# Kernel optimization log

Measured on AMD Instinct MI355X. Metric: run time of the kernel, lower is better.

Reference implementation:

```python
import jax, jax.numpy as jnp
import numpy as np

N = 50000
E = 1600000
D = 64


def setup_inputs() -> dict:
    key = jax.random.key(0)
    ks = jax.random.split(key, 12)
    glorot = lambda k, shape: jax.random.uniform(
        k, shape, jnp.float32, -1.0, 1.0) * (np.sqrt(2.0) * np.sqrt(6.0 / sum(shape)))
    return {
        "feat": jax.random.normal(ks[0], (N, D), jnp.float32),
        "norm": jax.random.uniform(ks[1], (N,), jnp.float32),
        "edge_src": jax.random.randint(ks[2], (E,), 0, N),
        "edge_dst": jax.random.randint(ks[3], (E,), 0, N),
        "etype": jax.random.randint(ks[4], (E,), 0, 4),
        "W_rel": glorot(ks[5], (D, D)),
        "lin_w": glorot(ks[6], (2 * D, 1)),
        "lin_b": jnp.zeros((1,), jnp.float32),
        "loop_w": glorot(ks[7], (D, D)),
        "evolve_loop_w": glorot(ks[8], (D, D)),
    }


def reference(feat, norm, edge_src, edge_dst, etype, W_rel, lin_w, lin_b,
              loop_w, evolve_loop_w):
    # --- message function: per-edge attention + per-edge matmul ---
    src = feat[edge_src]              # [E, D] gather
    dst = feat[edge_dst]              # [E, D] gather
    att_logit = jnp.concatenate([src, dst], axis=1) @ lin_w + lin_b  # [E, 1]
    atten = jax.nn.sigmoid(jax.nn.relu(att_logit[:, 0]))            # [E]
    # source code applies weight_relation to every edge-type bucket, so the
    # etype split+concat is a no-op permutation of messages
    msg = src @ W_rel                                                # [E, D]

    # --- reduce: attention-weighted mailbox sum (segment reduction) ---
    agg = jax.ops.segment_sum(atten[:, None] * msg, edge_dst, num_segments=N)
    indeg = jax.ops.segment_sum(jnp.ones((edge_dst.shape[0],), feat.dtype),
                                edge_dst, num_segments=N)            # [N]
    has_msg = (indeg > 0)[:, None]
    # DGL: zero in-degree nodes keep their old feat; apply_func scales by norm
    node_feat = jnp.where(has_msg, agg, feat) * norm[:, None]

    # --- self loop: loop_weight where in_degree>0, evolve_loop_weight else ---
    loop_msg = jnp.where(has_msg, feat @ loop_w, feat @ evolve_loop_w)

    return jnp.tanh(node_feat + loop_msg)
```

## Files before the change

### kernel.cpp

```cpp
#include <hip/hip_runtime.h>
#include <hip/hip_bf16.h>
#include <hip/hip_fp16.h>
#include <math.h>


#define D 64
#define SHIFT 6
#define NB (1 << SHIFT)
#define SCM 1024
#define CHUNK 4096
#define CAPB 2560
#define NPW 8

typedef _Float16 half8 __attribute__((ext_vector_type(8)));
typedef float f32x4 __attribute__((ext_vector_type(4)));

__global__ __launch_bounds__(256) void fused_pre(
    const float* __restrict__ feat, const float* __restrict__ W_rel,
    const float* __restrict__ lin_w, const float* __restrict__ lin_b,
    const float* __restrict__ loop_w, const float* __restrict__ evolve_w,
    float* __restrict__ s1, float* __restrict__ s2, __half* __restrict__ FWh,
    __half* __restrict__ WT, int N) {
  if (blockIdx.x == 0) {
    for (int i = threadIdx.x; i < 192 * 64; i += 256) {
      const int c192 = i >> 6, k = i & 63;
      const int m = c192 >> 6, c = c192 & 63;
      const float* Wm = (m == 0) ? W_rel : (m == 1) ? loop_w : evolve_w;
      WT[i] = __float2half(Wm[k * 64 + c]);
    }
  }

  const int lane = threadIdx.x & 63;
  const int w    = threadIdx.x >> 6;
  const int r    = lane & 15;
  const int g    = lane >> 4;
  const int m0   = (blockIdx.x * 4 + w) * 16;
  if (m0 >= N) return;

  half8 bw[4][2];
  half8 ba[2];
  #pragma unroll
  for (int ks = 0; ks < 2; ++ks) {
    #pragma unroll
    for (int j = 0; j < 8; ++j) {
      const int k = ks * 32 + g * 8 + j;
      #pragma unroll
      for (int nt = 0; nt < 4; ++nt)
        bw[nt][ks][j] = (_Float16)W_rel[k * 64 + nt * 16 + r];
      const float av = (r == 0) ? lin_w[k] : (r == 1) ? lin_w[64 + k] : 0.0f;
      ba[ks][j] = (_Float16)av;
    }
  }

  half8 ah[2], al[2];
  const int arow = m0 + r;
  #pragma unroll
  for (int ks = 0; ks < 2; ++ks) {
    float v[8];
    if (arow < N) {
      const float4 u0 = *(const float4*)&feat[(size_t)arow * D + ks * 32 + g * 8];
      const float4 u1 = *(const float4*)&feat[(size_t)arow * D + ks * 32 + g * 8 + 4];
      v[0] = u0.x; v[1] = u0.y; v[2] = u0.z; v[3] = u0.w;
      v[4] = u1.x; v[5] = u1.y; v[6] = u1.z; v[7] = u1.w;
    } else {
      #pragma unroll
      for (int q = 0; q < 8; ++q) v[q] = 0.0f;
    }
    #pragma unroll
    for (int q = 0; q < 8; ++q) {
      const _Float16 hh = (_Float16)v[q];
      ah[ks][q] = hh;
      al[ks][q] = (_Float16)(v[q] - (float)hh);
    }
  }

  #pragma unroll
  for (int nt = 0; nt < 4; ++nt) {
    f32x4 acc = {0.0f, 0.0f, 0.0f, 0.0f};
    #pragma unroll
    for (int ks = 0; ks < 2; ++ks) {
      acc = __builtin_amdgcn_mfma_f32_16x16x32_f16(ah[ks], bw[nt][ks], acc, 0, 0, 0);
      acc = __builtin_amdgcn_mfma_f32_16x16x32_f16(al[ks], bw[nt][ks], acc, 0, 0, 0);
    }
    #pragma unroll
    for (int q = 0; q < 4; ++q) {
      const int n = m0 + g * 4 + q;
      if (n < N) FWh[(size_t)n * D + nt * 16 + r] = __float2half(acc[q]);
    }
  }

  f32x4 acc5 = {0.0f, 0.0f, 0.0f, 0.0f};
  #pragma unroll
  for (int ks = 0; ks < 2; ++ks) {
    acc5 = __builtin_amdgcn_mfma_f32_16x16x32_f16(ah[ks], ba[ks], acc5, 0, 0, 0);
    acc5 = __builtin_amdgcn_mfma_f32_16x16x32_f16(al[ks], ba[ks], acc5, 0, 0, 0);
  }
  if (r < 2) {
    const float b = lin_b[0];
    #pragma unroll
    for (int q = 0; q < 4; ++q) {
      const int n = m0 + g * 4 + q;
      if (n < N) {
        if (r == 0) s1[n] = acc5[q] + b;
        else        s2[n] = acc5[q];
      }
    }
  }
}

__global__ __launch_bounds__(512) void coarse_scatter(
    const int* __restrict__ esrc, const int* __restrict__ edst,
    const float* __restrict__ s1, const float* __restrict__ s2,
    int* __restrict__ gcur, uint2* __restrict__ ebuf, int E, int C) {
  __shared__ int h[SCM];
  __shared__ int cur[SCM];
  __shared__ int bl[SCM];
  for (int i = threadIdx.x; i < C; i += 512) h[i] = 0;
  __syncthreads();
  const int E4 = E >> 2;
  const int4* edst4 = (const int4*)edst;
  const int4* esrc4 = (const int4*)esrc;
  const int b4 = blockIdx.x * (CHUNK >> 2);
  const bool tail0 = (blockIdx.x == 0) && (threadIdx.x == 0);

  #pragma unroll
  for (int k = 0; k < CHUNK / 2048; ++k) {
    const int i4 = b4 + threadIdx.x + 512 * k;
    if (i4 < E4) {
      const int4 d = edst4[i4];
      atomicAdd(&h[d.x >> SHIFT], 1);
      atomicAdd(&h[d.y >> SHIFT], 1);
      atomicAdd(&h[d.z >> SHIFT], 1);
      atomicAdd(&h[d.w >> SHIFT], 1);
    }
  }
  if (tail0) for (int e = E4 << 2; e < E; ++e) atomicAdd(&h[edst[e] >> SHIFT], 1);
  __syncthreads();
  for (int i = threadIdx.x; i < C; i += 512) {
    const int v = h[i];
    bl[i] = v ? atomicAdd(&gcur[i], v) : 0;
    cur[i] = 0;
  }
  __syncthreads();

  #pragma unroll
  for (int k = 0; k < CHUNK / 2048; ++k) {
    const int i4 = b4 + threadIdx.x + 512 * k;
    if (i4 < E4) {
      const int4 s = esrc4[i4];
      const int4 d = edst4[i4];
      const int ss[4] = {s.x, s.y, s.z, s.w};
      const int dd[4] = {d.x, d.y, d.z, d.w};
      float a1[4], a2[4];
      #pragma unroll
      for (int j = 0; j < 4; ++j) a1[j] = s1[ss[j]];
      #pragma unroll
      for (int j = 0; j < 4; ++j) a2[j] = s2[dd[j]];
      #pragma unroll
      for (int j = 0; j < 4; ++j) {
        const float a = 1.0f / (1.0f + __expf(-fmaxf(a1[j] + a2[j], 0.0f)));
        const int bk = dd[j] >> SHIFT;
        const int rr = atomicAdd(&cur[bk], 1);
        ebuf[(size_t)bk * CAPB + bl[bk] + rr] =
            make_uint2((unsigned)ss[j] | ((unsigned)(dd[j] & (NB - 1)) << 26),
                       __float_as_uint(a));
      }
    }
  }
  if (tail0) {
    for (int e = E4 << 2; e < E; ++e) {
      const int sj = esrc[e], dj = edst[e];
      const float a = 1.0f / (1.0f + __expf(-fmaxf(s1[sj] + s2[dj], 0.0f)));
      const int bk = dj >> SHIFT;
      const int rr = atomicAdd(&cur[bk], 1);
      ebuf[(size_t)bk * CAPB + bl[bk] + rr] =
          make_uint2((unsigned)sj | ((unsigned)(dj & (NB - 1)) << 26),
                     __float_as_uint(a));
    }
  }
}

__global__ __launch_bounds__(512, 4) void sort_reduce_finalize(
    const float* __restrict__ feat, const __half* __restrict__ FWh,
    const __half* __restrict__ WT, const float* __restrict__ norm,
    const int* __restrict__ gcur, const uint2* __restrict__ ebuf,
    float* __restrict__ out, int C, int N) {
  __shared__ uint2 sdata[CAPB];
  __shared__ float Yl[NB * D];
  __shared__ int hist[NB];
  __shared__ int starts[NB + 1];
  __shared__ int roff[NB];

  const int tid  = threadIdx.x;
  const int lane = tid & 63;
  const int w    = tid >> 6;
  const int b    = blockIdx.x;
  const int n0   = b << SHIFT;
  const int beg  = b * CAPB;
  const int cnt  = min(gcur[b], CAPB);

  if (tid < NB) hist[tid] = 0;
  __syncthreads();

  uint2 ereg[5];
  #pragma unroll
  for (int k = 0; k < 5; ++k) {
    const int i = tid + (k << 9);
    if (i < cnt) ereg[k] = ebuf[beg + i];
  }

  const int r = lane & 15, g = lane >> 4;
  const bool evw = (w >= 4);
  const int mt = w & 3;
  f32x4 ym[4];
  {
    half8 ah[2], al[2];
    const int arow = n0 + mt * 16 + r;
    #pragma unroll
    for (int ks = 0; ks < 2; ++ks) {
      float v[8];
      if (arow < N) {
        const float4 u0 = *(const float4*)&feat[(size_t)arow * D + ks * 32 + g * 8];
        const float4 u1 = *(const float4*)&feat[(size_t)arow * D + ks * 32 + g * 8 + 4];
        v[0] = u0.x; v[1] = u0.y; v[2] = u0.z; v[3] = u0.w;
        v[4] = u1.x; v[5] = u1.y; v[6] = u1.z; v[7] = u1.w;
      } else {
        #pragma unroll
        for (int q = 0; q < 8; ++q) v[q] = 0.0f;
      }
      #pragma unroll
      for (int q = 0; q < 8; ++q) {
        const _Float16 hh = (_Float16)v[q];
        ah[ks][q] = hh;
        al[ks][q] = (_Float16)(v[q] - (float)hh);
      }
    }
    const int wrow0 = evw ? 128 : 64;
    #pragma unroll
    for (int nt = 0; nt < 4; ++nt) {
      f32x4 a0 = {0.0f, 0.0f, 0.0f, 0.0f};
      #pragma unroll
      for (int ks = 0; ks < 2; ++ks) {
        const half8 bw = *reinterpret_cast<const half8*>(
            WT + (size_t)(wrow0 + nt * 16 + r) * 64 + ks * 32 + g * 8);
        a0 = __builtin_amdgcn_mfma_f32_16x16x32_f16(ah[ks], bw, a0, 0, 0, 0);
        a0 = __builtin_amdgcn_mfma_f32_16x16x32_f16(al[ks], bw, a0, 0, 0, 0);
      }
      ym[nt] = a0;
    }
  }

  #pragma unroll
  for (int k = 0; k < 5; ++k) {
    const int i = tid + (k << 9);
    if (i < cnt) atomicAdd(&hist[ereg[k].x >> 26], 1);
  }
  __syncthreads();
  if (tid < 64) {
    const int v = hist[tid];
    int incl = v;
    #pragma unroll
    for (int off = 1; off < 64; off <<= 1) {
      const int o = __shfl_up(incl, off, 64);
      if (tid >= off) incl += o;
    }
    starts[tid] = incl - v;
    roff[tid]   = incl - v;
    if (tid == 63) starts[64] = incl;
  }
  __syncthreads();
  #pragma unroll
  for (int k = 0; k < 5; ++k) {
    const int i = tid + (k << 9);
    if (i < cnt) {
      const int pos = atomicAdd(&roff[ereg[k].x >> 26], 1);
      sdata[pos] = ereg[k];
    }
  }
  #pragma unroll
  for (int nt = 0; nt < 4; ++nt) {
    #pragma unroll
    for (int q = 0; q < 4; ++q) {
      const int gr = mt * 16 + g * 4 + q;
      const bool hm = starts[gr + 1] > starts[gr];
      if (evw != hm) Yl[gr * D + nt * 16 + r] = ym[nt][q];
    }
  }
  __syncthreads();

  float agg[NPW];
  #pragma unroll
  for (int j = 0; j < NPW; ++j) agg[j] = 0.0f;
  for (int j = 0; j < NPW; ++j) {
    const int dl = w * NPW + j;
    const int n  = n0 + dl;
    if (n >= N) break;
    const int rb = __builtin_amdgcn_readfirstlane(starts[dl]);
    const int re = __builtin_amdgcn_readfirstlane(starts[dl + 1]);
    float a = 0.0f;
    int p = rb;
    for (; p + 16 <= re; p += 16) {
      uint2 ee[16];
      #pragma unroll
      for (int q = 0; q < 16; ++q) ee[q] = sdata[p + q];
      float ff[16];
      #pragma unroll
      for (int q = 0; q < 16; ++q)
        ff[q] = __half2float(FWh[(size_t)(ee[q].x & 0x03FFFFFFu) * D + lane]);
      #pragma unroll
      for (int q = 0; q < 16; ++q) a += __uint_as_float(ee[q].y) * ff[q];
    }
    for (; p + 4 <= re; p += 4) {
      uint2 ee[4];
      #pragma unroll
      for (int q = 0; q < 4; ++q) ee[q] = sdata[p + q];
      #pragma unroll
      for (int q = 0; q < 4; ++q)
        a += __uint_as_float(ee[q].y) *
             __half2float(FWh[(size_t)(ee[q].x & 0x03FFFFFFu) * D + lane]);
    }
    for (; p < re; ++p) {
      const uint2 en = sdata[p];
      a += __uint_as_float(en.y) *
           __half2float(FWh[(size_t)(en.x & 0x03FFFFFFu) * D + lane]);
    }
    agg[j] = a;
  }

  for (int j = 0; j < NPW; ++j) {
    const int dl = w * NPW + j;
    const int n  = n0 + dl;
    if (n >= N) break;
    const bool hm = starts[dl + 1] > starts[dl];
    const float nr = norm[n];
    const float base = hm ? agg[j] : feat[(size_t)n * D + lane];
    out[(size_t)n * D + lane] = tanhf(base * nr + Yl[dl * D + lane]);
  }
}

extern "C" void kernel_launch(void* const* d_in, const int* in_sizes, int n_in,
                              void* d_out, int out_size, void* d_ws, size_t ws_size,
                              hipStream_t stream) {
  const float* feat     = (const float*)d_in[0];
  const float* norm     = (const float*)d_in[1];
  const int*   esrc     = (const int*)d_in[2];
  const int*   edst     = (const int*)d_in[3];
  const float* W_rel    = (const float*)d_in[5];
  const float* lin_w    = (const float*)d_in[6];
  const float* lin_b    = (const float*)d_in[7];
  const float* loop_w   = (const float*)d_in[8];
  const float* evolve_w = (const float*)d_in[9];
  float* out = (float*)d_out;

  const int N = in_sizes[1];
  const int E = in_sizes[2];
  const int C = (N + NB - 1) >> SHIFT;

  char* p = (char*)d_ws;
  float*  s1     = (float*)p;   p += (size_t)N * sizeof(float);
  float*  s2     = (float*)p;   p += (size_t)N * sizeof(float);
  int*    gcur   = (int*)p;     p += (size_t)2048 * sizeof(int);
  __half* WT     = (__half*)p;  p += (size_t)192 * 64 * sizeof(__half);
  __half* FWh    = (__half*)p;  p += (size_t)N * D * sizeof(__half);
  uint2*  ebuf   = (uint2*)p;

  const int eblocks = (E + CHUNK - 1) / CHUNK;
  const int mblocks = (N + 63) / 64;

  hipMemsetAsync(gcur, 0, (size_t)C * sizeof(int), stream);
  fused_pre<<<mblocks, 256, 0, stream>>>(feat, W_rel, lin_w, lin_b,
                                         loop_w, evolve_w,
                                         s1, s2, FWh, WT, N);
  coarse_scatter<<<eblocks, 512, 0, stream>>>(esrc, edst, s1, s2, gcur,
                                              ebuf, E, C);
  sort_reduce_finalize<<<C, 512, 0, stream>>>(feat, FWh, WT, norm,
                                              gcur, ebuf, out, C, N);
}
```

Before: 189.9 us.

## Halve scatter chunk, skip unneeded evolve matmul, gather two edges per wave

Coarse scatter now processes one int4 per thread (CHUNK 2048), so twice as many blocks each handle half the edges. In the reduce kernel the edge-buffer load is fused with the histogram, and the evolve-weight MFMA is skipped for waves whose 16 nodes all have in-edges. The aggregation loop splits the wave into halves that each gather a different edge, reading two fp16 features per lane as a half2 and combining the halves with shuffles. This cuts gather instructions and redundant matmul work, at the cost of extra shuffles and less parallelism for the tail edges.

New measurement: 181.9 us. 1.04x faster.

```diff
diff --git a/kernel.cpp b/kernel.cpp
--- a/kernel.cpp
+++ b/kernel.cpp
@@ -8,7 +8,7 @@
 #define SHIFT 6
 #define NB (1 << SHIFT)
 #define SCM 1024
-#define CHUNK 4096
+#define CHUNK 2048
 #define CAPB 2560
 #define NPW 8
 
@@ -120,19 +120,15 @@
   const int E4 = E >> 2;
   const int4* edst4 = (const int4*)edst;
   const int4* esrc4 = (const int4*)esrc;
-  const int b4 = blockIdx.x * (CHUNK >> 2);
+  const int i4 = blockIdx.x * 512 + threadIdx.x;
   const bool tail0 = (blockIdx.x == 0) && (threadIdx.x == 0);
 
-  #pragma unroll
-  for (int k = 0; k < CHUNK / 2048; ++k) {
-    const int i4 = b4 + threadIdx.x + 512 * k;
-    if (i4 < E4) {
-      const int4 d = edst4[i4];
-      atomicAdd(&h[d.x >> SHIFT], 1);
-      atomicAdd(&h[d.y >> SHIFT], 1);
-      atomicAdd(&h[d.z >> SHIFT], 1);
-      atomicAdd(&h[d.w >> SHIFT], 1);
-    }
+  if (i4 < E4) {
+    const int4 d = edst4[i4];
+    atomicAdd(&h[d.x >> SHIFT], 1);
+    atomicAdd(&h[d.y >> SHIFT], 1);
+    atomicAdd(&h[d.z >> SHIFT], 1);
+    atomicAdd(&h[d.w >> SHIFT], 1);
   }
   if (tail0) for (int e = E4 << 2; e < E; ++e) atomicAdd(&h[edst[e] >> SHIFT], 1);
   __syncthreads();
@@ -143,28 +139,24 @@
   }
   __syncthreads();
 
-  #pragma unroll
-  for (int k = 0; k < CHUNK / 2048; ++k) {
-    const int i4 = b4 + threadIdx.x + 512 * k;
-    if (i4 < E4) {
-      const int4 s = esrc4[i4];
-      const int4 d = edst4[i4];
-      const int ss[4] = {s.x, s.y, s.z, s.w};
-      const int dd[4] = {d.x, d.y, d.z, d.w};
-      float a1[4], a2[4];
-      #pragma unroll
-      for (int j = 0; j < 4; ++j) a1[j] = s1[ss[j]];
-      #pragma unroll
-      for (int j = 0; j < 4; ++j) a2[j] = s2[dd[j]];
-      #pragma unroll
-      for (int j = 0; j < 4; ++j) {
-        const float a = 1.0f / (1.0f + __expf(-fmaxf(a1[j] + a2[j], 0.0f)));
-        const int bk = dd[j] >> SHIFT;
-        const int rr = atomicAdd(&cur[bk], 1);
-        ebuf[(size_t)bk * CAPB + bl[bk] + rr] =
-            make_uint2((unsigned)ss[j] | ((unsigned)(dd[j] & (NB - 1)) << 26),
-                       __float_as_uint(a));
-      }
+  if (i4 < E4) {
+    const int4 s = esrc4[i4];
+    const int4 d = edst4[i4];
+    const int ss[4] = {s.x, s.y, s.z, s.w};
+    const int dd[4] = {d.x, d.y, d.z, d.w};
+    float a1[4], a2[4];
+    #pragma unroll
+    for (int j = 0; j < 4; ++j) a1[j] = s1[ss[j]];
+    #pragma unroll
+    for (int j = 0; j < 4; ++j) a2[j] = s2[dd[j]];
+    #pragma unroll
+    for (int j = 0; j < 4; ++j) {
+      const float a = 1.0f / (1.0f + __expf(-fmaxf(a1[j] + a2[j], 0.0f)));
+      const int bk = dd[j] >> SHIFT;
+      const int rr = atomicAdd(&cur[bk], 1);
+      ebuf[(size_t)bk * CAPB + bl[bk] + rr] =
+          make_uint2((unsigned)ss[j] | ((unsigned)(dd[j] & (NB - 1)) << 26),
+                     __float_as_uint(a));
     }
   }
   if (tail0) {
@@ -206,54 +198,10 @@
   #pragma unroll
   for (int k = 0; k < 5; ++k) {
     const int i = tid + (k << 9);
-    if (i < cnt) ereg[k] = ebuf[beg + i];
-  }
-
-  const int r = lane & 15, g = lane >> 4;
-  const bool evw = (w >= 4);
-  const int mt = w & 3;
-  f32x4 ym[4];
-  {
-    half8 ah[2], al[2];
-    const int arow = n0 + mt * 16 + r;
-    #pragma unroll
-    for (int ks = 0; ks < 2; ++ks) {
-      float v[8];
-      if (arow < N) {
-        const float4 u0 = *(const float4*)&feat[(size_t)arow * D + ks * 32 + g * 8];
-        const float4 u1 = *(const float4*)&feat[(size_t)arow * D + ks * 32 + g * 8 + 4];
-        v[0] = u0.x; v[1] = u0.y; v[2] = u0.z; v[3] = u0.w;
-        v[4] = u1.x; v[5] = u1.y; v[6] = u1.z; v[7] = u1.w;
-      } else {
-        #pragma unroll
-        for (int q = 0; q < 8; ++q) v[q] = 0.0f;
-      }
-      #pragma unroll
-      for (int q = 0; q < 8; ++q) {
-        const _Float16 hh = (_Float16)v[q];
-        ah[ks][q] = hh;
-        al[ks][q] = (_Float16)(v[q] - (float)hh);
-      }
-    }
-    const int wrow0 = evw ? 128 : 64;
-    #pragma unroll
-    for (int nt = 0; nt < 4; ++nt) {
-      f32x4 a0 = {0.0f, 0.0f, 0.0f, 0.0f};
-      #pragma unroll
-      for (int ks = 0; ks < 2; ++ks) {
-        const half8 bw = *reinterpret_cast<const half8*>(
-            WT + (size_t)(wrow0 + nt * 16 + r) * 64 + ks * 32 + g * 8);
-        a0 = __builtin_amdgcn_mfma_f32_16x16x32_f16(ah[ks], bw, a0, 0, 0, 0);
-        a0 = __builtin_amdgcn_mfma_f32_16x16x32_f16(al[ks], bw, a0, 0, 0, 0);
-      }
-      ym[nt] = a0;
-    }
-  }
-
-  #pragma unroll
-  for (int k = 0; k < 5; ++k) {
-    const int i = tid + (k << 9);
-    if (i < cnt) atomicAdd(&hist[ereg[k].x >> 26], 1);
+    if (i < cnt) {
+      ereg[k] = ebuf[beg + i];
+      atomicAdd(&hist[ereg[k].x >> 26], 1);
+    }
   }
   __syncthreads();
   if (tid < 64) {
@@ -277,17 +225,64 @@
       sdata[pos] = ereg[k];
     }
   }
-  #pragma unroll
-  for (int nt = 0; nt < 4; ++nt) {
-    #pragma unroll
-    for (int q = 0; q < 4; ++q) {
-      const int gr = mt * 16 + g * 4 + q;
-      const bool hm = starts[gr + 1] > starts[gr];
-      if (evw != hm) Yl[gr * D + nt * 16 + r] = ym[nt][q];
-    }
-  }
-  __syncthreads();
-
+
+  {
+    const int r = lane & 15, g = lane >> 4;
+    const bool evw = (w >= 4);
+    const int mt = w & 3;
+    bool skip = false;
+    if (evw) {
+      const int rr0 = mt * 16;
+      const int flag = (lane < 16)
+          ? ((starts[rr0 + lane + 1] > starts[rr0 + lane]) ? 1 : 0) : 1;
+      skip = (__ballot(flag == 0) == 0ULL);
+    }
+    if (!skip) {
+      half8 ah[2], al[2];
+      const int arow = n0 + mt * 16 + r;
+      #pragma unroll
+      for (int ks = 0; ks < 2; ++ks) {
+        float v[8];
+        if (arow < N) {
+          const float4 u0 = *(const float4*)&feat[(size_t)arow * D + ks * 32 + g * 8];
+          const float4 u1 = *(const float4*)&feat[(size_t)arow * D + ks * 32 + g * 8 + 4];
+          v[0] = u0.x; v[1] = u0.y; v[2] = u0.z; v[3] = u0.w;
+          v[4] = u1.x; v[5] = u1.y; v[6] = u1.z; v[7] = u1.w;
+        } else {
+          #pragma unroll
+          for (int q = 0; q < 8; ++q) v[q] = 0.0f;
+        }
+        #pragma unroll
+        for (int q = 0; q < 8; ++q) {
+          const _Float16 hh = (_Float16)v[q];
+          ah[ks][q] = hh;
+          al[ks][q] = (_Float16)(v[q] - (float)hh);
+        }
+      }
+      const int wrow0 = evw ? 128 : 64;
+      #pragma unroll
+      for (int nt = 0; nt < 4; ++nt) {
+        f32x4 a0 = {0.0f, 0.0f, 0.0f, 0.0f};
+        #pragma unroll
+        for (int ks = 0; ks < 2; ++ks) {
+          const half8 bw = *reinterpret_cast<const half8*>(
+              WT + (size_t)(wrow0 + nt * 16 + r) * 64 + ks * 32 + g * 8);
+          a0 = __builtin_amdgcn_mfma_f32_16x16x32_f16(ah[ks], bw, a0, 0, 0, 0);
+          a0 = __builtin_amdgcn_mfma_f32_16x16x32_f16(al[ks], bw, a0, 0, 0, 0);
+        }
+        #pragma unroll
+        for (int q = 0; q < 4; ++q) {
+          const int gr = mt * 16 + g * 4 + q;
+          const bool hm = starts[gr + 1] > starts[gr];
+          if (evw != hm) Yl[gr * D + nt * 16 + r] = a0[q];
+        }
+      }
+    }
+  }
+  __syncthreads();
+
+  const int half = lane >> 5;
+  const int hc   = lane & 31;
   float agg[NPW];
   #pragma unroll
   for (int j = 0; j < NPW; ++j) agg[j] = 0.0f;
@@ -297,34 +292,36 @@
     if (n >= N) break;
     const int rb = __builtin_amdgcn_readfirstlane(starts[dl]);
     const int re = __builtin_amdgcn_readfirstlane(starts[dl + 1]);
-    float a = 0.0f;
+    float sa = 0.0f, sb = 0.0f;
     int p = rb;
     for (; p + 16 <= re; p += 16) {
-      uint2 ee[16];
-      #pragma unroll
-      for (int q = 0; q < 16; ++q) ee[q] = sdata[p + q];
-      float ff[16];
-      #pragma unroll
-      for (int q = 0; q < 16; ++q)
-        ff[q] = __half2float(FWh[(size_t)(ee[q].x & 0x03FFFFFFu) * D + lane]);
-      #pragma unroll
-      for (int q = 0; q < 16; ++q) a += __uint_as_float(ee[q].y) * ff[q];
-    }
-    for (; p + 4 <= re; p += 4) {
-      uint2 ee[4];
-      #pragma unroll
-      for (int q = 0; q < 4; ++q) ee[q] = sdata[p + q];
-      #pragma unroll
-      for (int q = 0; q < 4; ++q)
-        a += __uint_as_float(ee[q].y) *
-             __half2float(FWh[(size_t)(ee[q].x & 0x03FFFFFFu) * D + lane]);
-    }
-    for (; p < re; ++p) {
-      const uint2 en = sdata[p];
-      a += __uint_as_float(en.y) *
-           __half2float(FWh[(size_t)(en.x & 0x03FFFFFFu) * D + lane]);
-    }
-    agg[j] = a;
+      uint2 ee[8];
+      #pragma unroll
+      for (int q = 0; q < 8; ++q) ee[q] = sdata[p + 2 * q + half];
+      #pragma unroll
+      for (int q = 0; q < 8; ++q) {
+        const uint vv = *(const uint*)(
+            FWh + (((size_t)(ee[q].x & 0x03FFFFFFu)) << 6) + (hc << 1));
+        const float a = __uint_as_float(ee[q].y);
+        const float2 f2 = __half22float2(*(const __half2*)&vv);
+        sa += a * f2.x; sb += a * f2.y;
+      }
+    }
+    for (; p < re; p += 2) {
+      const int idx = p + half;
+      const bool vld = idx < re;
+      const uint2 e = sdata[vld ? idx : rb];
+      const uint vv = *(const uint*)(
+          FWh + (((size_t)(e.x & 0x03FFFFFFu)) << 6) + (hc << 1));
+      const float a = vld ? __uint_as_float(e.y) : 0.0f;
+      const float2 f2 = __half22float2(*(const __half2*)&vv);
+      sa += a * f2.x; sb += a * f2.y;
+    }
+    sa += __shfl_xor(sa, 32, 64);
+    sb += __shfl_xor(sb, 32, 64);
+    const float t0 = __shfl(sa, lane >> 1, 64);
+    const float t1 = __shfl(sb, lane >> 1, 64);
+    agg[j] = (lane & 1) ? t1 : t0;
   }
 
   for (int j = 0; j < NPW; ++j) {
```
